# Kernel optimization log

Measured on AMD Instinct MI355X. Metric: run time of the kernel, lower is better.

## Reference

```python
import jax, jax.numpy as jnp
import numpy as np

B, S, D, H = 2, 2048, 2048, 16
DH = D // H  # 128
EPS = 1e-6


def _rms_norm(x, w):
    # RMSNorm over last dim with learnable scale
    var = jnp.mean(jnp.square(x), axis=-1, keepdims=True)
    return x * jax.lax.rsqrt(var + EPS) * w


def _apply_rope(x, angles):
    # x: [B, S, H, DH]; angles: [S, DH//2]; interleaved pair rotation
    xs = x.reshape(*x.shape[:-1], DH // 2, 2)
    x0, x1 = xs[..., 0], xs[..., 1]
    cos = jnp.cos(angles)[None, :, None, :]  # [1,S,1,DH/2]
    sin = jnp.sin(angles)[None, :, None, :]
    r0 = x0 * cos - x1 * sin
    r1 = x0 * sin + x1 * cos
    return jnp.stack([r0, r1], axis=-1).reshape(x.shape)


def setup_inputs() -> dict:
    key = jax.random.key(0)
    ks = jax.random.split(key, 4)
    x = jax.random.normal(ks[0], (B, S, D), dtype=jnp.float32)
    # standard RoPE angle table: pos * inv_freq
    inv_freq = 1.0 / (10000.0 ** (jnp.arange(0, DH, 2, dtype=jnp.float32) / DH))
    pos = jnp.arange(S, dtype=jnp.float32)
    rp_freqs = pos[:, None] * inv_freq[None, :]  # [S, DH/2]
    Win = jax.random.normal(ks[1], (3 * D, D), dtype=jnp.float32) * (D ** -0.5)
    b_in = jnp.zeros((3 * D,), dtype=jnp.float32)
    Wout = jax.random.normal(ks[2], (D, D), dtype=jnp.float32) * (D ** -0.5)
    b_out = jnp.zeros((D,), dtype=jnp.float32)
    qk_w = jnp.ones((DH,), dtype=jnp.float32)
    out_w = jnp.ones((D,), dtype=jnp.float32)
    return {"x": x, "rp_freqs": rp_freqs, "Win": Win, "b_in": b_in,
            "Wout": Wout, "b_out": b_out, "qk_w": qk_w, "out_w": out_w}


def reference(x, rp_freqs, Win, b_in, Wout, b_out, qk_w, out_w):
    b, s, d = x.shape
    qkv = jnp.einsum('bsd,ed->bse', x, Win) + b_in  # [B,S,3D]
    qkv = qkv.reshape(b, s, 3, H, DH)
    q, k, v = qkv[:, :, 0], qkv[:, :, 1], qkv[:, :, 2]  # each [B,S,H,DH]
    q = _apply_rope(q, rp_freqs)
    k = _apply_rope(k, rp_freqs)
    q = _rms_norm(q, qk_w)
    k = _rms_norm(k, qk_w)
    # causal SDPA, scale = 1/sqrt(DH) (default)
    a = jax.nn.dot_product_attention(q, k, v, is_causal=True)  # [B,S,H,DH]
    a = a.reshape(b, s, d)
    a = _rms_norm(a, out_w)
    return jnp.einsum('bsd,ed->bse', a, Wout) + b_out
```

## Files before the change

kernel.cpp:

```cpp
#include <hip/hip_runtime.h>
#include <cstdint>
#include <cstddef>

#define Bq  2
#define Sq  2048
#define Dq  2048
#define Hq  16
#define DHq 128
#define E3q 6144

typedef __attribute__((ext_vector_type(8))) short s16x8;
typedef __attribute__((ext_vector_type(4))) float f32x4;

__device__ __forceinline__ unsigned short f2bf(float f){
  union { float f; unsigned u; } v; v.f = f;
  unsigned r = v.u + 0x7FFFu + ((v.u >> 16) & 1u);
  return (unsigned short)(r >> 16);
}
__device__ __forceinline__ float bf2f(unsigned short b){
  union { unsigned u; float f; } v; v.u = ((unsigned)b) << 16;
  return v.f;
}
__device__ __forceinline__ unsigned cvtpk_bf16(float lo, float hi){
  unsigned r;
  asm("v_cvt_pk_bf16_f32 %0, %1, %2" : "=v"(r) : "v"(lo), "v"(hi));
  return r;
}

__device__ __forceinline__ void gload_lds16(const void* g, void* l){
  __builtin_amdgcn_global_load_lds(
      (const __attribute__((address_space(1))) void*)g,
      (__attribute__((address_space(3))) void*)l, 16, 0, 0);
}

__global__ __launch_bounds__(256) void k_convert3(const float* __restrict__ x,
                                                  const float* __restrict__ win,
                                                  const float* __restrict__ wout,
                                                  const float* __restrict__ out_w,
                                                  const float* __restrict__ rp,
                                                  unsigned short* __restrict__ xb,
                                                  unsigned short* __restrict__ wb,
                                                  unsigned short* __restrict__ woutb,
                                                  float2* __restrict__ rpcs){
  const int NX = (Bq*Sq*Dq)/4;
  const int NW = (E3q*Dq)/4;
  const int NO = (Dq*Dq)/4;
  const int NR = (Sq*64)/4;
  const int total = NX + NW + NO + NR;
  int stride = gridDim.x * blockDim.x;
  for (int i = blockIdx.x*blockDim.x + threadIdx.x; i < total; i += stride){
    if (i < NX + NW){
      const float* src; unsigned short* dst; int j;
      if (i < NX){ src = x; dst = xb; j = i; }
      else { src = win; dst = wb; j = i - NX; }
      float4 v = reinterpret_cast<const float4*>(src)[j];
      ushort4 o;
      o.x = f2bf(v.x); o.y = f2bf(v.y); o.z = f2bf(v.z); o.w = f2bf(v.w);
      reinterpret_cast<ushort4*>(dst)[j] = o;
    } else if (i < NX + NW + NO){
      int j = i - NX - NW;
      float4 v = reinterpret_cast<const float4*>(wout)[j];
      float4 w = reinterpret_cast<const float4*>(out_w)[j & 511];
      ushort4 o;
      o.x = f2bf(v.x*w.x); o.y = f2bf(v.y*w.y); o.z = f2bf(v.z*w.z); o.w = f2bf(v.w*w.w);
      reinterpret_cast<ushort4*>(woutb)[j] = o;
    } else {
      int j = i - NX - NW - NO;
      float4 a = reinterpret_cast<const float4*>(rp)[j];
      float sn0,cs0,sn1,cs1,sn2,cs2,sn3,cs3;
      sincosf(a.x,&sn0,&cs0); sincosf(a.y,&sn1,&cs1);
      sincosf(a.z,&sn2,&cs2); sincosf(a.w,&sn3,&cs3);
      float4 p0 = make_float4(cs0,sn0,cs1,sn1);
      float4 p1 = make_float4(cs2,sn2,cs3,sn3);
      reinterpret_cast<float4*>(rpcs)[j*2  ] = p0;
      reinterpret_cast<float4*>(rpcs)[j*2+1] = p1;
    }
  }
}

__global__ __launch_bounds__(512, 1) void k_gemm1f(const unsigned short* __restrict__ A,
                                                   const unsigned short* __restrict__ Bt,
                                                   const float* __restrict__ bias,
                                                   const float2* __restrict__ rpcs,
                                                   const float* __restrict__ qk_w,
                                                   unsigned short* __restrict__ Qp,
                                                   unsigned short* __restrict__ Kp,
                                                   unsigned short* __restrict__ Vt){
  const int K = 2048, NI = 16;
  const int bid = blockIdx.x;
  const int xcd = bid & 7, u = bid >> 3;
  const int m0 = (xcd*4 + (u & 3)) * 128;
  const int n0 = (u >> 2) * 256;

  const int tid = threadIdx.x;
  const int lane = tid & 63, w = tid >> 6, g = lane >> 4, c = lane & 15;
  const int wm = w >> 2, wn = w & 3;

  __shared__ __align__(16) unsigned short L[49152];

  const int srow = tid >> 2, spc = tid & 3;
  const int ssw = (spc ^ ((srow >> 1) & 3)) << 3;
  const unsigned short* aSrc  = A  + (size_t)(m0 + srow      )*K + ssw;
  const unsigned short* bSrc0 = Bt + (size_t)(n0 + srow      )*K + ssw;
  const unsigned short* bSrc1 = Bt + (size_t)(n0 + srow + 128)*K + ssw;

  auto stA = [&](int t, int h){
    gload_lds16(aSrc + t*64 + h*32, &L[((t&1)*2 + h)*4096 + tid*8]);
  };
  auto stB = [&](int t, int h, int uu){
    const unsigned short* s = (uu==0) ? bSrc0 : bSrc1;
    gload_lds16(s + t*64 + h*32, &L[16384 + ((t&1)*2 + h)*8192 + uu*4096 + tid*8]);
  };

  int aoff[4], boff[4];
#pragma unroll
  for (int mf=0; mf<4; ++mf){
    int row = wm*64 + mf*16 + c;
    aoff[mf] = row*32 + ((g ^ ((row>>1)&3)) << 3);
  }
#pragma unroll
  for (int nf=0; nf<4; ++nf){
    int row = wn*64 + nf*16 + c;
    boff[nf] = row*32 + ((g ^ ((row>>1)&3)) << 3);
  }

  f32x4 acc[4][4];
#pragma unroll
  for (int i=0;i<4;i++)
#pragma unroll
    for (int j=0;j<4;j++)
#pragma unroll
      for (int r=0;r<4;r++) acc[i][j][r] = 0.f;

  auto RDA = [&](int b, int h, s16x8* af){
    const int ab = (b*2 + h)*4096;
#pragma unroll
    for (int mf=0; mf<4; ++mf) af[mf] = *(const s16x8*)&L[ab + aoff[mf]];
  };
  auto RDB = [&](int b, int h, int nh, s16x8* bf){
    const int bb = 16384 + (b*2 + h)*8192;
#pragma unroll
    for (int j=0; j<2; ++j) bf[j] = *(const s16x8*)&L[bb + boff[nh*2 + j]];
  };
  auto MM = [&](s16x8* af, s16x8* bf, int nh){
    __builtin_amdgcn_s_setprio(1);
#pragma unroll
    for (int mf=0; mf<4; ++mf)
#pragma unroll
      for (int j=0; j<2; ++j)
        acc[mf][nh*2+j] = __builtin_amdgcn_mfma_f32_16x16x32_bf16(af[mf], bf[j], acc[mf][nh*2+j], 0,0,0);
    __builtin_amdgcn_s_setprio(0);
  };
  auto BAR = [&](){
    __builtin_amdgcn_sched_barrier(0);
    __builtin_amdgcn_s_barrier();
    __builtin_amdgcn_sched_barrier(0);
  };

  stA(0,0); stB(0,0,0); stB(0,0,1);
  stA(0,1); stB(0,1,0); stB(0,1,1);
  stA(1,0); stB(1,0,0); stB(1,0,1);
  asm volatile("s_waitcnt vmcnt(3)" ::: "memory");
  __builtin_amdgcn_s_barrier();

  for (int i=0; i<NI; ++i){
    const int T0 = 2*i, T1 = 2*i + 1;
    const bool st = (i < NI-1);
    s16x8 af[4], bf[2];
    RDA(0,0,af); RDB(0,0,0,bf);
    stA(T1,1); stB(T1,1,0);
    BAR(); MM(af,bf,0); BAR();
    RDB(0,0,1,bf);
    stB(T1,1,1);
    BAR(); MM(af,bf,1); BAR();
    RDA(0,1,af); RDB(0,1,0,bf);
    if (st){ stA(T0+2,0); stB(T0+2,0,0); }
    BAR(); MM(af,bf,0); BAR();
    RDB(0,1,1,bf);
    if (st){ stB(T0+2,0,1); }
    __builtin_amdgcn_sched_barrier(0);
    if (st) asm volatile("s_waitcnt vmcnt(3)" ::: "memory");
    else    asm volatile("s_waitcnt vmcnt(0)" ::: "memory");
    BAR(); MM(af,bf,1); BAR();
    RDA(1,0,af); RDB(1,0,0,bf);
    if (st){ stA(T0+2,1); stB(T0+2,1,0); }
    BAR(); MM(af,bf,0); BAR();
    RDB(1,0,1,bf);
    if (st){ stB(T0+2,1,1); }
    BAR(); MM(af,bf,1); BAR();
    RDA(1,1,af); RDB(1,1,0,bf);
    if (st){ stA(T1+2,0); stB(T1+2,0,0); }
    BAR(); MM(af,bf,0); BAR();
    RDB(1,1,1,bf);
    if (st){ stB(T1+2,0,1); }
    __builtin_amdgcn_sched_barrier(0);
    if (st) asm volatile("s_waitcnt vmcnt(3)" ::: "memory");
    else    asm volatile("s_waitcnt vmcnt(0)" ::: "memory");
    BAR(); MM(af,bf,1); BAR();
  }

  const int btype = (n0 < 2048) ? 0 : (n0 < 4096) ? 1 : 2;
  const int b  = m0 >> 11;
  const int sb = m0 & 2047;
  const int h0 = (n0 & 2047) >> 7;
  const int LTS = 264;
  const float QSCALE = 0.08838834764831845f * 1.4426950408889634f;

#pragma unroll
  for (int nf=0; nf<4; ++nf){
    const float bv = bias[n0 + wn*64 + nf*16 + c];
#pragma unroll
    for (int mf=0; mf<4; ++mf)
#pragma unroll
      for (int r=0; r<4; ++r) acc[mf][nf][r] += bv;
  }

  __syncthreads();

  if (btype < 2){
    float s2[4][4];
#pragma unroll
    for (int mf=0;mf<4;mf++)
#pragma unroll
      for (int r=0;r<4;r++){
        float s = 0.f;
#pragma unroll
        for (int nf=0;nf<4;nf++){ float v = acc[mf][nf][r]; s += v*v; }
        s2[mf][r] = s;
      }
#pragma unroll
    for (int m=1;m<16;m<<=1)
#pragma unroll
      for (int mf=0;mf<4;mf++)
#pragma unroll
        for (int r=0;r<4;r++) s2[mf][r] += __shfl_xor(s2[mf][r], m);
    float* Ssum = (float*)&L[0];
    if (c==0 && (wn&1)==0){
#pragma unroll
      for (int mf=0;mf<4;mf++)
#pragma unroll
        for (int r=0;r<4;r++)
          Ssum[(wm*64+mf*16+g*4+r)*2 + (wn>>1)] = s2[mf][r];
    }
    __syncthreads();
    if (c==0 && (wn&1)==1){
#pragma unroll
      for (int mf=0;mf<4;mf++)
#pragma unroll
        for (int r=0;r<4;r++)
          Ssum[(wm*64+mf*16+g*4+r)*2 + (wn>>1)] += s2[mf][r];
    }
    __syncthreads();
    float rsc[4][4];
#pragma unroll
    for (int mf=0;mf<4;mf++)
#pragma unroll
      for (int r=0;r<4;r++)
        rsc[mf][r] = rsqrtf(Ssum[(wm*64+mf*16+g*4+r)*2 + (wn>>1)]*(1.f/128.f) + 1e-6f);
    __syncthreads();

    const float qmul = (btype==0) ? QSCALE : 1.f;
    float wq[4];
    int pp[4];
#pragma unroll
    for (int nf=0;nf<4;nf++){
      wq[nf] = qk_w[(wn*64+nf*16+c)&127];
      pp[nf] = ((wn*64+nf*16+c)&127) >> 1;
    }

#pragma unroll
    for (int mf=0;mf<4;mf++)
#pragma unroll
      for (int r=0;r<4;r++){
        const int rowl = wm*64+mf*16+g*4+r;
        const int s = sb + rowl;
        const float sc = rsc[mf][r] * qmul;
#pragma unroll
        for (int nf=0;nf<4;nf++){
          float2 t = rpcs[s*64 + pp[nf]];
          float v  = acc[mf][nf][r];
          float pv = __shfl_xor(v, 1);
          float rot = ((c&1)==0) ? (v*t.x - pv*t.y) : (pv*t.y + v*t.x);
          L[rowl*LTS + wn*64+nf*16+c] = f2bf(rot * sc * wq[nf]);
        }
      }
    __syncthreads();
    {
      const int rw = tid >> 2, hd = (tid>>1)&1, hf = tid&1;
      const int bh = b*Hq + h0 + hd;
      unsigned short* dst = ((btype==0) ? Qp : Kp)
                          + ((size_t)bh*Sq + sb + rw)*DHq + hf*64;
      const unsigned short* srcl = &L[rw*LTS + hd*128 + hf*64];
#pragma unroll
      for (int i2=0;i2<8;i2++)
        *(s16x8*)&dst[i2*8] = *(const s16x8*)&srcl[i2*8];
    }
  } else {
#pragma unroll
    for (int mf=0;mf<4;mf++)
#pragma unroll
      for (int r=0;r<4;r++){
        const int rowl = wm*64+mf*16+g*4+r;
#pragma unroll
        for (int nf=0;nf<4;nf++)
          L[rowl*LTS + wn*64+nf*16+c] = f2bf(acc[mf][nf][r]);
      }
    __syncthreads();
    {
      const int dh2 = tid >> 1, hfr = (tid & 1) * 64;
      const int hd = dh2 >> 7, dh = dh2 & 127;
      const int bh = b*Hq + h0 + hd;
      unsigned short buf[64];
#pragma unroll
      for (int i2=0;i2<64;i2++) buf[i2] = L[(hfr+i2)*LTS + dh2];
      unsigned short* dst = Vt + ((size_t)bh*DHq + dh)*Sq + sb + hfr;
#pragma unroll
      for (int i2=0;i2<8;i2++)
        *(s16x8*)&dst[i2*8] = *(const s16x8*)&buf[i2*8];
    }
  }
}

__global__ __launch_bounds__(512, 1) void k_gemm2_8ph(const unsigned short* __restrict__ A,
                                                      const unsigned short* __restrict__ Bt,
                                                      const float* __restrict__ bias,
                                                      const float* __restrict__ rscale,
                                                      float* __restrict__ C){
  const int K = 2048, N = 2048, NI = 16;
  const int bid = blockIdx.x;
  const int xcd = bid & 7, u = bid >> 3;
  const int m0 = (xcd*4 + (u & 3)) * 128;
  const int n0 = (u >> 2) * 256;

  const int tid = threadIdx.x;
  const int lane = tid & 63, w = tid >> 6, g = lane >> 4, c = lane & 15;
  const int wm = w >> 2, wn = w & 3;

  __shared__ __align__(16) unsigned short L[49152];

  const int srow = tid >> 2, spc = tid & 3;
  const int ssw = (spc ^ ((srow >> 1) & 3)) << 3;
  const unsigned short* aSrc  = A  + (size_t)(m0 + srow      )*K + ssw;
  const unsigned short* bSrc0 = Bt + (size_t)(n0 + srow      )*K + ssw;
  const unsigned short* bSrc1 = Bt + (size_t)(n0 + srow + 128)*K + ssw;

  auto stA = [&](int t, int h){
    gload_lds16(aSrc + t*64 + h*32, &L[((t&1)*2 + h)*4096 + tid*8]);
  };
  auto stB = [&](int t, int h, int uu){
    const unsigned short* s = (uu==0) ? bSrc0 : bSrc1;
    gload_lds16(s + t*64 + h*32, &L[16384 + ((t&1)*2 + h)*8192 + uu*4096 + tid*8]);
  };

  int aoff[4], boff[4];
#pragma unroll
  for (int mf=0; mf<4; ++mf){
    int row = wm*64 + mf*16 + c;
    aoff[mf] = row*32 + ((g ^ ((row>>1)&3)) << 3);
  }
#pragma unroll
  for (int nf=0; nf<4; ++nf){
    int row = wn*64 + nf*16 + c;
    boff[nf] = row*32 + ((g ^ ((row>>1)&3)) << 3);
  }

  f32x4 acc[4][4];
#pragma unroll
  for (int i=0;i<4;i++)
#pragma unroll
    for (int j=0;j<4;j++)
#pragma unroll
      for (int r=0;r<4;r++) acc[i][j][r] = 0.f;

  auto RDA = [&](int b, int h, s16x8* af){
    const int ab = (b*2 + h)*4096;
#pragma unroll
    for (int mf=0; mf<4; ++mf) af[mf] = *(const s16x8*)&L[ab + aoff[mf]];
  };
  auto RDB = [&](int b, int h, int nh, s16x8* bf){
    const int bb = 16384 + (b*2 + h)*8192;
#pragma unroll
    for (int j=0; j<2; ++j) bf[j] = *(const s16x8*)&L[bb + boff[nh*2 + j]];
  };
  auto MM = [&](s16x8* af, s16x8* bf, int nh){
    __builtin_amdgcn_s_setprio(1);
#pragma unroll
    for (int mf=0; mf<4; ++mf)
#pragma unroll
      for (int j=0; j<2; ++j)
        acc[mf][nh*2+j] = __builtin_amdgcn_mfma_f32_16x16x32_bf16(af[mf], bf[j], acc[mf][nh*2+j], 0,0,0);
    __builtin_amdgcn_s_setprio(0);
  };
  auto BAR = [&](){
    __builtin_amdgcn_sched_barrier(0);
    __builtin_amdgcn_s_barrier();
    __builtin_amdgcn_sched_barrier(0);
  };

  stA(0,0); stB(0,0,0); stB(0,0,1);
  stA(0,1); stB(0,1,0); stB(0,1,1);
  stA(1,0); stB(1,0,0); stB(1,0,1);
  asm volatile("s_waitcnt vmcnt(3)" ::: "memory");
  __builtin_amdgcn_s_barrier();

  for (int i=0; i<NI; ++i){
    const int T0 = 2*i, T1 = 2*i + 1;
    const bool st = (i < NI-1);
    s16x8 af[4], bf[2];
    RDA(0,0,af); RDB(0,0,0,bf);
    stA(T1,1); stB(T1,1,0);
    BAR(); MM(af,bf,0); BAR();
    RDB(0,0,1,bf);
    stB(T1,1,1);
    BAR(); MM(af,bf,1); BAR();
    RDA(0,1,af); RDB(0,1,0,bf);
    if (st){ stA(T0+2,0); stB(T0+2,0,0); }
    BAR(); MM(af,bf,0); BAR();
    RDB(0,1,1,bf);
    if (st){ stB(T0+2,0,1); }
    __builtin_amdgcn_sched_barrier(0);
    if (st) asm volatile("s_waitcnt vmcnt(3)" ::: "memory");
    else    asm volatile("s_waitcnt vmcnt(0)" ::: "memory");
    BAR(); MM(af,bf,1); BAR();
    RDA(1,0,af); RDB(1,0,0,bf);
    if (st){ stA(T0+2,1); stB(T0+2,1,0); }
    BAR(); MM(af,bf,0); BAR();
    RDB(1,0,1,bf);
    if (st){ stB(T0+2,1,1); }
    BAR(); MM(af,bf,1); BAR();
    RDA(1,1,af); RDB(1,1,0,bf);
    if (st){ stA(T1+2,0); stB(T1+2,0,0); }
    BAR(); MM(af,bf,0); BAR();
    RDB(1,1,1,bf);
    if (st){ stB(T1+2,0,1); }
    __builtin_amdgcn_sched_barrier(0);
    if (st) asm volatile("s_waitcnt vmcnt(3)" ::: "memory");
    else    asm volatile("s_waitcnt vmcnt(0)" ::: "memory");
    BAR(); MM(af,bf,1); BAR();
  }

#pragma unroll
  for (int nf=0; nf<4; ++nf){
    const int col = n0 + wn*64 + nf*16 + c;
    const float bv = bias[col];
#pragma unroll
    for (int mf=0; mf<4; ++mf){
      const int row = m0 + wm*64 + mf*16 + g*4;
#pragma unroll
      for (int r=0; r<4; ++r)
        C[(size_t)(row+r)*N + col] = acc[mf][nf][r]*rscale[row+r] + bv;
    }
  }
}

__global__ __launch_bounds__(256) void k_rowscale(const unsigned short* __restrict__ A,
                                                  float* __restrict__ sc){
  const int row = blockIdx.x;
  const int tid = threadIdx.x;
  s16x8 v = *(const s16x8*)&A[(size_t)row*Dq + tid*8];
  float ss = 0.f;
#pragma unroll
  for (int i=0;i<8;i++){ float f = bf2f((unsigned short)v[i]); ss += f*f; }
#pragma unroll
  for (int m=1;m<64;m<<=1) ss += __shfl_xor(ss, m);
  __shared__ float red[4];
  if ((tid&63)==0) red[tid>>6] = ss;
  __syncthreads();
  if (tid==0){
    float t = red[0]+red[1]+red[2]+red[3];
    sc[row] = rsqrtf(t*(1.f/2048.f) + 1e-6f);
  }
}

__global__ __launch_bounds__(256, 2) void k_attn(const unsigned short* __restrict__ Qp,
                                                 const unsigned short* __restrict__ Kp,
                                                 const unsigned short* __restrict__ Vt,
                                                 unsigned short* __restrict__ Ar){
  const int L = blockIdx.x;
  const int xcdL = L & 7, j = L >> 3;
  const int bh = xcdL*4 + ((j & 31) >> 3);
  const int qtile = (j < 32) ? (8 + (j & 7)) : (7 - (j & 7));
  const int b = bh >> 4, h = bh & 15;
  const int tid = threadIdx.x;
  const int w = tid >> 6, lane = tid & 63, g = lane >> 4, c = lane & 15;
  const int r0w = qtile*128 + w*32;

  const unsigned short* Qh = Qp + (size_t)bh * Sq * DHq;
  const unsigned short* Kh = Kp + (size_t)bh * Sq * DHq;
  const unsigned short* Vh = Vt + (size_t)bh * DHq * Sq;

  __shared__ __align__(16) unsigned short Ks[2][64*128];
  __shared__ __align__(16) unsigned short Vs[2][128*64];
  __shared__ __align__(16) unsigned short Pl[4][32*64];
  unsigned short* Pw = &Pl[w][0];

  s16x8 qf[2][4];
#pragma unroll
  for (int mi=0;mi<2;mi++)
#pragma unroll
    for (int kc=0;kc<4;kc++)
      qf[mi][kc] = *(const s16x8*)&Qh[(size_t)(r0w + mi*16 + c)*DHq + kc*32 + g*8];

  f32x4 acc[2][8];
#pragma unroll
  for (int mi=0;mi<2;mi++)
#pragma unroll
    for (int dt=0;dt<8;dt++)
#pragma unroll
      for (int r=0;r<4;r++) acc[mi][dt][r] = 0.f;
  float m_r[2] = { -INFINITY, -INFINITY };
  float l_p[2] = { 0.f, 0.f };

  const int nsteps = 2*qtile + 2;

  auto stage = [&](int j0s, int bufi){
#pragma unroll
    for (int i=0;i<4;i++){
      int pk = tid + i*256;
      int row = pk>>4, pcc = pk&15;
      gload_lds16(&Kh[(size_t)(j0s+row)*DHq + ((pcc^(row&7))<<3)], &Ks[bufi][pk*8]);
    }
#pragma unroll
    for (int i=0;i<4;i++){
      int pk = tid + i*256;
      int row = pk>>3, pcc = pk&7;
      gload_lds16(&Vh[(size_t)row*Sq + j0s + ((pcc^(row&7))<<3)], &Vs[bufi][pk*8]);
    }
  };

  stage(0, 0);
  __syncthreads();

  for (int t=0; t<nsteps; ++t){
    const int j0 = t*64;
    if (t+1 < nsteps) stage((t+1)*64, (t+1)&1);

    if (j0 <= r0w + 31){
      const unsigned short* Kc = &Ks[t&1][0];
      const unsigned short* Vc = &Vs[t&1][0];

      f32x4 sv[2][4];
#pragma unroll
      for (int mi=0;mi<2;mi++)
#pragma unroll
        for (int js=0;js<4;js++)
#pragma unroll
          for (int r=0;r<4;r++) sv[mi][js][r] = 0.f;

      __builtin_amdgcn_s_setprio(1);
#pragma unroll
      for (int js=0;js<4;js++){
        s16x8 kf[4];
#pragma unroll
        for (int kc=0;kc<4;kc++)
          kf[kc] = *(const s16x8*)&Kc[(js*16 + c)*128 + (((kc*4+g)^(c&7))<<3)];
#pragma unroll
        for (int mi=0;mi<2;mi++)
#pragma unroll
          for (int kc=0;kc<4;kc++)
            sv[mi][js] = __builtin_amdgcn_mfma_f32_16x16x32_bf16(kf[kc], qf[mi][kc], sv[mi][js], 0,0,0);
      }
      __builtin_amdgcn_s_setprio(0);

      if (j0 + 63 > r0w){
#pragma unroll
        for (int mi=0;mi<2;mi++){
          const int q = r0w + mi*16 + c;
#pragma unroll
          for (int js=0;js<4;js++)
#pragma unroll
            for (int r=0;r<4;r++)
              if (j0 + js*16 + g*4 + r > q) sv[mi][js][r] = -INFINITY;
        }
      }

      float pmx[2];
#pragma unroll
      for (int mi=0;mi<2;mi++){
        float mx = fmaxf(fmaxf(sv[mi][0][0],sv[mi][0][1]), fmaxf(sv[mi][0][2],sv[mi][0][3]));
#pragma unroll
        for (int js=1;js<4;js++){
          float a = fmaxf(fmaxf(sv[mi][js][0],sv[mi][js][1]), fmaxf(sv[mi][js][2],sv[mi][js][3]));
          mx = fmaxf(mx, a);
        }
        mx = fmaxf(mx, __shfl_xor(mx, 16));
        mx = fmaxf(mx, __shfl_xor(mx, 32));
        pmx[mi] = mx;
      }
      int need = (pmx[0] > m_r[0] + 8.f) | (pmx[1] > m_r[1] + 8.f);
      if (__any(need)){
#pragma unroll
        for (int mi=0;mi<2;mi++){
          float mnew = fmaxf(m_r[mi], pmx[mi]);
          float corr = exp2f(m_r[mi] - mnew);
          l_p[mi] *= corr;
          m_r[mi] = mnew;
#pragma unroll
          for (int dt=0;dt<8;dt++)
#pragma unroll
            for (int r=0;r<4;r++) acc[mi][dt][r] *= corr;
        }
      }
#pragma unroll
      for (int mi=0;mi<2;mi++){
        const float mm = m_r[mi];
        const int rowoff = (mi*16 + c)*64;
#pragma unroll
        for (int js=0;js<4;js++){
          float e0 = exp2f(sv[mi][js][0] - mm);
          float e1 = exp2f(sv[mi][js][1] - mm);
          float e2 = exp2f(sv[mi][js][2] - mm);
          float e3 = exp2f(sv[mi][js][3] - mm);
          l_p[mi] += (e0+e1)+(e2+e3);
          uint2 pk2;
          pk2.x = cvtpk_bf16(e0, e1);
          pk2.y = cvtpk_bf16(e2, e3);
          const int kc8 = js*2 + (g>>1);
          *(uint2*)&Pw[rowoff + ((kc8 ^ (c&7))<<3) + (g&1)*4] = pk2;
        }
      }

      s16x8 pfr[2][2];
#pragma unroll
      for (int mi=0;mi<2;mi++)
#pragma unroll
        for (int kc=0;kc<2;kc++)
          pfr[mi][kc] = *(const s16x8*)&Pw[(mi*16 + c)*64 + (((kc*4+g)^(c&7))<<3)];
      __builtin_amdgcn_s_setprio(1);
#pragma unroll
      for (int dt=0; dt<8; dt++){
#pragma unroll
        for (int kc=0;kc<2;kc++){
          s16x8 vfr = *(const s16x8*)&Vc[(dt*16 + c)*64 + (((kc*4+g)^(c&7))<<3)];
#pragma unroll
          for (int mi=0;mi<2;mi++)
            acc[mi][dt] = __builtin_amdgcn_mfma_f32_16x16x32_bf16(vfr, pfr[mi][kc], acc[mi][dt], 0,0,0);
        }
      }
      __builtin_amdgcn_s_setprio(0);
    }
    __syncthreads();
  }

#pragma unroll
  for (int mi=0;mi<2;mi++){
    float l = l_p[mi];
    l += __shfl_xor(l, 16);
    l += __shfl_xor(l, 32);
    const float inv = 1.f / l;
    const int row = r0w + mi*16 + c;
    unsigned short* dst = &Ar[((size_t)(b*Sq + row))*Dq + h*DHq];
#pragma unroll
    for (int dt=0; dt<8; dt++){
      uint2 o2;
      o2.x = cvtpk_bf16(acc[mi][dt][0]*inv, acc[mi][dt][1]*inv);
      o2.y = cvtpk_bf16(acc[mi][dt][2]*inv, acc[mi][dt][3]*inv);
      *(uint2*)&dst[dt*16 + g*4] = o2;
    }
  }
}

extern "C" void kernel_launch(void* const* d_in, const int* in_sizes, int n_in,
                              void* d_out, int out_size, void* d_ws, size_t ws_size,
                              hipStream_t stream){
  const float* x     = (const float*)d_in[0];
  const float* rp    = (const float*)d_in[1];
  const float* Win   = (const float*)d_in[2];
  const float* b_in  = (const float*)d_in[3];
  const float* Wout  = (const float*)d_in[4];
  const float* b_out = (const float*)d_in[5];
  const float* qk_w  = (const float*)d_in[6];
  const float* out_w = (const float*)d_in[7];
  float* outp = (float*)d_out;

  if (ws_size < (160ull<<20)) return;

  char* ws = (char*)d_ws;
  unsigned short* Xb    = (unsigned short*)(ws);
  unsigned short* Wb    = (unsigned short*)(ws + (16ull<<20));
  unsigned short* Woutb = (unsigned short*)(ws + (40ull<<20));
  float*          rsc   = (float*)         (ws + (48ull<<20));
  float2*         rpcs  = (float2*)        (ws + (49ull<<20));
  unsigned short* Qp    = (unsigned short*)(ws + (96ull<<20));
  unsigned short* Kp    = (unsigned short*)(ws + (112ull<<20));
  unsigned short* Vt    = (unsigned short*)(ws + (128ull<<20));
  unsigned short* Ar    = (unsigned short*)(ws + (144ull<<20));

  k_convert3<<<2048, 256, 0, stream>>>(x, Win, Wout, out_w, rp, Xb, Wb, Woutb, rpcs);
  k_gemm1f<<<768, 512, 0, stream>>>(Xb, Wb, b_in, rpcs, qk_w, Qp, Kp, Vt);
  k_attn<<<512, 256, 0, stream>>>(Qp, Kp, Vt, Ar);
  k_rowscale<<<Bq*Sq, 256, 0, stream>>>(Ar, rsc);
  k_gemm2_8ph<<<256, 512, 0, stream>>>(Ar, Woutb, b_out, rsc, outp);
}
```

Before: 266.4 us.

## Fuse output RMSNorm row statistics into attention and out-projection epilogues

The attention epilogue now computes the per-head sum of squares of each normalized output row and writes one float per row and head. The second GEMM epilogue adds up these 16 partials per row, forms the rsqrt scale in shared memory and applies it. This removes the separate row-scale kernel, its extra pass over the bf16 attention output and one launch. The statistics now come from fp32 values taken before bf16 rounding, so results differ slightly, and the GEMM gains a small epilogue with two extra barriers.

```diff
diff --git a/kernel.cpp b/kernel.cpp
--- a/kernel.cpp
+++ b/kernel.cpp
@@ -324,7 +324,7 @@
 __global__ __launch_bounds__(512, 1) void k_gemm2_8ph(const unsigned short* __restrict__ A,
                                                       const unsigned short* __restrict__ Bt,
                                                       const float* __restrict__ bias,
-                                                      const float* __restrict__ rscale,
+                                                      const float* __restrict__ ssqp,
                                                       float* __restrict__ C){
   const int K = 2048, N = 2048, NI = 16;
   const int bid = blockIdx.x;
@@ -439,43 +439,36 @@
     BAR(); MM(af,bf,1); BAR();
   }
 
+  __syncthreads();
+  float* SS = (float*)&L[0];
+  if (tid < 128){
+    const float* p = ssqp + (size_t)(m0 + tid)*16;
+    float s = 0.f;
+#pragma unroll
+    for (int h=0; h<16; ++h) s += p[h];
+    SS[tid] = rsqrtf(s*(1.f/2048.f) + 1e-6f);
+  }
+  __syncthreads();
+
 #pragma unroll
   for (int nf=0; nf<4; ++nf){
     const int col = n0 + wn*64 + nf*16 + c;
     const float bv = bias[col];
 #pragma unroll
     for (int mf=0; mf<4; ++mf){
-      const int row = m0 + wm*64 + mf*16 + g*4;
+      const int rowl = wm*64 + mf*16 + g*4;
 #pragma unroll
       for (int r=0; r<4; ++r)
-        C[(size_t)(row+r)*N + col] = acc[mf][nf][r]*rscale[row+r] + bv;
-    }
-  }
-}
-
-__global__ __launch_bounds__(256) void k_rowscale(const unsigned short* __restrict__ A,
-                                                  float* __restrict__ sc){
-  const int row = blockIdx.x;
-  const int tid = threadIdx.x;
-  s16x8 v = *(const s16x8*)&A[(size_t)row*Dq + tid*8];
-  float ss = 0.f;
-#pragma unroll
-  for (int i=0;i<8;i++){ float f = bf2f((unsigned short)v[i]); ss += f*f; }
-#pragma unroll
-  for (int m=1;m<64;m<<=1) ss += __shfl_xor(ss, m);
-  __shared__ float red[4];
-  if ((tid&63)==0) red[tid>>6] = ss;
-  __syncthreads();
-  if (tid==0){
-    float t = red[0]+red[1]+red[2]+red[3];
-    sc[row] = rsqrtf(t*(1.f/2048.f) + 1e-6f);
+        C[(size_t)(m0+rowl+r)*N + col] = acc[mf][nf][r]*SS[rowl+r] + bv;
+    }
   }
 }
 
 __global__ __launch_bounds__(256, 2) void k_attn(const unsigned short* __restrict__ Qp,
                                                  const unsigned short* __restrict__ Kp,
                                                  const unsigned short* __restrict__ Vt,
-                                                 unsigned short* __restrict__ Ar){
+                                                 unsigned short* __restrict__ Ar,
+                                                 float* __restrict__ ssqp){
   const int L = blockIdx.x;
   const int xcdL = L & 7, j = L >> 3;
   const int bh = xcdL*4 + ((j & 31) >> 3);
@@ -650,13 +643,21 @@
     const float inv = 1.f / l;
     const int row = r0w + mi*16 + c;
     unsigned short* dst = &Ar[((size_t)(b*Sq + row))*Dq + h*DHq];
+    float sq = 0.f;
 #pragma unroll
     for (int dt=0; dt<8; dt++){
+      float v0 = acc[mi][dt][0]*inv, v1 = acc[mi][dt][1]*inv;
+      float v2 = acc[mi][dt][2]*inv, v3 = acc[mi][dt][3]*inv;
+      sq += v0*v0 + v1*v1 + v2*v2 + v3*v3;
       uint2 o2;
-      o2.x = cvtpk_bf16(acc[mi][dt][0]*inv, acc[mi][dt][1]*inv);
-      o2.y = cvtpk_bf16(acc[mi][dt][2]*inv, acc[mi][dt][3]*inv);
+      o2.x = cvtpk_bf16(v0, v1);
+      o2.y = cvtpk_bf16(v2, v3);
       *(uint2*)&dst[dt*16 + g*4] = o2;
     }
+    sq += __shfl_xor(sq, 16);
+    sq += __shfl_xor(sq, 32);
+    if (g == 0)
+      ssqp[(size_t)(b*Sq + row)*16 + h] = sq;
   }
 }
 
@@ -679,7 +680,7 @@
   unsigned short* Xb    = (unsigned short*)(ws);
   unsigned short* Wb    = (unsigned short*)(ws + (16ull<<20));
   unsigned short* Woutb = (unsigned short*)(ws + (40ull<<20));
-  float*          rsc   = (float*)         (ws + (48ull<<20));
+  float*          ssqp  = (float*)         (ws + (48ull<<20));
   float2*         rpcs  = (float2*)        (ws + (49ull<<20));
   unsigned short* Qp    = (unsigned short*)(ws + (96ull<<20));
   unsigned short* Kp    = (unsigned short*)(ws + (112ull<<20));
@@ -688,7 +689,6 @@
 
   k_convert3<<<2048, 256, 0, stream>>>(x, Win, Wout, out_w, rp, Xb, Wb, Woutb, rpcs);
   k_gemm1f<<<768, 512, 0, stream>>>(Xb, Wb, b_in, rpcs, qk_w, Qp, Kp, Vt);
-  k_attn<<<512, 256, 0, stream>>>(Qp, Kp, Vt, Ar);
-  k_rowscale<<<Bq*Sq, 256, 0, stream>>>(Ar, rsc);
-  k_gemm2_8ph<<<256, 512, 0, stream>>>(Ar, Woutb, b_out, rsc, outp);
-}
+  k_attn<<<512, 256, 0, stream>>>(Qp, Kp, Vt, Ar, ssqp);
+  k_gemm2_8ph<<<256, 512, 0, stream>>>(Ar, Woutb, b_out, ssqp, outp);
+}
```

Result: no change. 262.0 us, median of 2 (-1.7%).
